# Kernel tuning notes

Measured on AMD Instinct MI355X. Metric: run time of the kernel, lower is better.

## Reference

```python
import jax, jax.numpy as jnp
import numpy as np

B, DIN, F, H, C = 8192, 2048, 2048, 2048, 345
EPS = 1e-5


def setup_inputs() -> dict:
    key = jax.random.key(0)
    ks = jax.random.split(key, 8)
    rng = np.random.default_rng(0)
    # labels and sort order (torch.sort is stable here via argsort kind='stable')
    y_np = rng.integers(0, C, size=B).astype(np.int64)
    order_np = np.argsort(y_np, kind='stable')
    ys = y_np[order_np]
    # per-class random permutations within each sorted segment (torch.randperm per interval)
    shuf1 = np.empty(B, dtype=np.int64)
    shuf2 = np.empty(B, dtype=np.int64)
    for c in np.unique(ys):
        idx = np.nonzero(ys == c)[0]
        shuf1[idx] = rng.permutation(idx)
        shuf2[idx] = rng.permutation(idx)
    s = 0.02  # weight init scale
    return {
        'x': jax.random.normal(ks[0], (B, DIN), jnp.float32),
        'lam': jnp.array([float(rng.beta(0.5, 0.5))], jnp.float32),
        'Wf': jax.random.normal(ks[1], (DIN, F), jnp.float32) * s,
        'bf': jnp.zeros((F,), jnp.float32),
        'W1': jax.random.normal(ks[2], (F, H), jnp.float32) * s,
        'b1': jnp.zeros((H,), jnp.float32),
        'g1': jnp.ones((H,), jnp.float32),
        'be1': jnp.zeros((H,), jnp.float32),
        'W2': jax.random.normal(ks[3], (H, H), jnp.float32) * s,
        'b2': jnp.zeros((H,), jnp.float32),
        'g2': jnp.ones((H,), jnp.float32),
        'be2': jnp.zeros((H,), jnp.float32),
        'W3': jax.random.normal(ks[4], (H, F), jnp.float32) * s,
        'b3': jnp.zeros((F,), jnp.float32),
        'g3': jnp.ones((F,), jnp.float32),
        'be3': jnp.zeros((F,), jnp.float32),
        'Wc': jax.random.normal(ks[5], (F, C), jnp.float32) * s,
        'bc': jnp.zeros((C,), jnp.float32),
        'y': jnp.asarray(y_np),
        'order': jnp.asarray(order_np),
        'shuf1': jnp.asarray(shuf1),
        'shuf2': jnp.asarray(shuf2),
    }


def _bn(x, g, b):
    # BatchNorm1d, training mode: biased batch stats
    m = jnp.mean(x, axis=0)
    v = jnp.var(x, axis=0)
    return (x - m) * jax.lax.rsqrt(v + EPS) * g + b


def reference(x, lam, Wf, bf, W1, b1, g1, be1, W2, b2, g2, be2, W3, b3, g3, be3, Wc, bc, y, order, shuf1, shuf2):
    lam = lam[0]
    xs = x[order]           # sorted-by-label gather (vectorized)
    ys = y[order]
    feat = jax.nn.relu(xs @ Wf + bf)                      # featurizer
    h = jax.nn.relu(_bn(feat @ W1 + b1, g1, be1))         # cdpl projector
    h = jax.nn.relu(_bn(h @ W2 + b2, g2, be2))
    proj = _bn(h @ W3 + b3, g3, be3)
    out = feat @ Wc + bc                                  # classifier logits
    out2, feat2 = out[shuf1], proj[shuf1]                 # per-class shuffles
    out3, feat3 = out[shuf2], proj[shuf2]
    out3 = lam * out2 + (1.0 - lam) * out3
    feat3 = lam * feat2 + (1.0 - lam) * feat3
    mse = lambda a, b: jnp.mean((a - b) ** 2)
    L_ind_logit = mse(out, out2)
    L_hdl_logit = mse(out, out3)
    L_ind_feat = 0.3 * mse(proj, feat2)
    L_hdl_feat = 0.3 * mse(proj, feat3)
    logp = jax.nn.log_softmax(out, axis=-1)
    cl_loss = -jnp.mean(jnp.take_along_axis(logp, ys[:, None], axis=-1))
    C_scale = jax.lax.stop_gradient(jnp.minimum(cl_loss, 1.0))  # .item() -> constant
    loss = cl_loss + C_scale * (lam * (L_ind_logit + L_ind_feat) + (1.0 - lam) * (L_hdl_logit + L_hdl_feat))
    return loss
```

## Files before the change

### kernel.cpp

```cpp
#include <hip/hip_runtime.h>

#define NB   8192
#define NF   2048
#define NC   345
#define NCP  384
#define EPSV 1e-5f

#define SX   (5.75f / 127.0f)
#define SW   (0.115f / 127.0f)
#define SF   (5.2f / 127.0f)
#define SH   (5.75f / 127.0f)
#define ST1  (3.34f / 127.0f)
#define ST2  (3.68f / 127.0f)
#define QX   (1.0f / SX)
#define QW   (1.0f / SW)
#define QF   (1.0f / SF)
#define QH   (1.0f / SH)
#define QT1  (1.0f / ST1)
#define QT2  (1.0f / ST2)

typedef __bf16 bf16x8 __attribute__((ext_vector_type(8)));
typedef float  f32x4  __attribute__((ext_vector_type(4)));
typedef int    i32x4  __attribute__((ext_vector_type(4)));

__device__ __forceinline__ float bs2f(unsigned int u) { return __uint_as_float(u << 16); }
__device__ __forceinline__ unsigned short f2bs(float f) {
    unsigned int u = __float_as_uint(f);
    u += 0x7fffu + ((u >> 16) & 1u);
    return (unsigned short)(u >> 16);
}
__device__ __forceinline__ int q8i(float v, float iq) {
    int t = __float2int_rn(v * iq);
    return t > 127 ? 127 : (t < -127 ? -127 : t);
}

#define GLD16(g, l)                                                                     \
    __builtin_amdgcn_global_load_lds((const __attribute__((address_space(1))) void*)(g),\
                                     (__attribute__((address_space(3))) void*)(l),      \
                                     16, 0, 0)

__global__ void k_gather(const float* __restrict__ x, const int* __restrict__ order,
                         char* __restrict__ xq) {
    const int row = blockIdx.x;
    const long src = order[row];
    const float4* xr = (const float4*)(x + src * 2048);
    float4 a = xr[threadIdx.x * 2 + 0];
    float4 b = xr[threadIdx.x * 2 + 1];
    unsigned int lo = (unsigned)(q8i(a.x, QX) & 255) | ((unsigned)(q8i(a.y, QX) & 255) << 8) |
                      ((unsigned)(q8i(a.z, QX) & 255) << 16) | ((unsigned)(q8i(a.w, QX) & 255) << 24);
    unsigned int hi = (unsigned)(q8i(b.x, QX) & 255) | ((unsigned)(q8i(b.y, QX) & 255) << 8) |
                      ((unsigned)(q8i(b.z, QX) & 255) << 16) | ((unsigned)(q8i(b.w, QX) & 255) << 24);
    uint2 o; o.x = lo; o.y = hi;
    ((uint2*)(xq + (long)row * 2048))[threadIdx.x] = o;
}

__global__ void k_transpose4(const float* __restrict__ W0, const float* __restrict__ W1,
                             const float* __restrict__ W2, const float* __restrict__ W3,
                             char* __restrict__ Wt) {
    __shared__ float tile[32][33];
    const float* Wz = (blockIdx.z == 0) ? W0 : (blockIdx.z == 1) ? W1
                     : (blockIdx.z == 2) ? W2 : W3;
    char* out = Wt + (size_t)blockIdx.z * 2048 * 2048;
    const int n0 = blockIdx.x * 32, k0 = blockIdx.y * 32;
    const int tx = threadIdx.x, ty = threadIdx.y;
    #pragma unroll
    for (int i = 0; i < 32; i += 8)
        tile[ty + i][tx] = Wz[(long)(k0 + ty + i) * 2048 + n0 + tx];
    __syncthreads();
    #pragma unroll
    for (int i = 0; i < 32; i += 8)
        out[(long)(n0 + ty + i) * 2048 + k0 + tx] = (char)q8i(tile[tx][ty + i], QW);
}

__global__ void k_transposeC(const float* __restrict__ W, char* __restrict__ Wt8,
                             int K, int N, int Npad) {
    __shared__ float tile[32][33];
    const int n0 = blockIdx.x * 32, k0 = blockIdx.y * 32;
    const int tx = threadIdx.x, ty = threadIdx.y;
    #pragma unroll
    for (int i = 0; i < 32; i += 8) {
        int n = n0 + tx, k = k0 + ty + i;
        tile[ty + i][tx] = (n < N) ? W[(long)k * N + n] : 0.f;
    }
    __syncthreads();
    #pragma unroll
    for (int i = 0; i < 32; i += 8) {
        int n = n0 + ty + i, k = k0 + tx;
        if (n < Npad) Wt8[(long)n * K + k] = (char)q8i(tile[tx][ty + i], QW);
    }
}

__global__ void k_padbias(const float* __restrict__ bc, float* __restrict__ bcp) {
    const int i = threadIdx.x + blockIdx.x * blockDim.x;
    if (i < NCP) bcp[i] = (i < NC) ? bc[i] : 0.f;
}

#define BARX  do { asm volatile("" ::: "memory"); __builtin_amdgcn_s_barrier(); \
                   asm volatile("" ::: "memory"); } while (0)
#define LGKM0 asm volatile("s_waitcnt lgkmcnt(0)" ::: "memory")
#define VMW4  asm volatile("s_waitcnt vmcnt(4)" ::: "memory")
#define VMW0  asm volatile("s_waitcnt vmcnt(0)" ::: "memory")

#define RDX(u, AV, BV) do {                                                            \
    const char* A_ = &L[((u) & 3) * 32768];                                            \
    const char* B_ = A_ + 16384;                                                       \
    _Pragma("unroll") for (int m_ = 0; m_ < 8; m_++)                                   \
        AV[m_] = *(const i32x4*)&A_[(wm * 128 + m_ * 16 + frow) * 64 + slt];           \
    _Pragma("unroll") for (int n_ = 0; n_ < 4; n_++)                                   \
        BV[n_] = *(const i32x4*)&B_[(wn * 64 + n_ * 16 + frow) * 64 + slt];            \
} while (0)

#define MMX(AV, BV) do {                                                               \
    __builtin_amdgcn_s_setprio(1);                                                     \
    _Pragma("unroll") for (int n_ = 0; n_ < 4; n_++)                                   \
    _Pragma("unroll") for (int m_ = 0; m_ < 8; m_++)                                   \
        acc[m_][n_] = __builtin_amdgcn_mfma_i32_16x16x64_i8(BV[n_], AV[m_],            \
                                                            acc[m_][n_], 0, 0, 0);    \
    __builtin_amdgcn_s_setprio(0);                                                     \
} while (0)

template <int RELU, int STATS>
__global__ __launch_bounds__(512, 2) void k_gemmq(
    const char* __restrict__ A,
    const char* __restrict__ Bt,
    const float* __restrict__ bias,
    char* __restrict__ C8,
    float* __restrict__ stats,
    float S, float IQ, int N, int K) {
    __shared__ char L[4 * 32768];
    const int tid  = threadIdx.x;
    const int lane = tid & 63;
    const int wv   = tid >> 6;
    const int frow = lane & 15;
    const int kg   = lane >> 4;
    const int wm   = wv >> 2;
    const int wn   = wv & 3;
    const int slt  = (kg ^ ((frow >> 1) & 3)) * 16;

    const int id  = blockIdx.x;
    const int xcd = id & 7, kid = id >> 3;
    const int brow = (xcd * 4 + (kid & 3)) * 256;
    const int bcol = (kid >> 2) * 256;

    const char* pA[2];
    const char* pB[2];
    #pragma unroll
    for (int i = 0; i < 2; i++) {
        const int q = tid + i * 512;
        const int j = q >> 2;
        const int c = (q & 3) ^ ((j >> 1) & 3);
        pA[i] = A  + (long)(brow + j) * K + c * 16;
        pB[i] = Bt + (long)(bcol + j) * K + c * 16;
    }

    i32x4 acc[8][4];
    #pragma unroll
    for (int m = 0; m < 8; m++)
        #pragma unroll
        for (int n = 0; n < 4; n++)
            #pragma unroll
            for (int r = 0; r < 4; r++) acc[m][n][r] = 0;

    auto stage = [&](int s) {
        char* Lb = &L[(s & 3) * 32768];
        const int ko = s * 64;
        GLD16(pA[0] + ko, Lb + wv * 1024);
        GLD16(pA[1] + ko, Lb + 8192 + wv * 1024);
        GLD16(pB[0] + ko, Lb + 16384 + wv * 1024);
        GLD16(pB[1] + ko, Lb + 24576 + wv * 1024);
    };

    i32x4 avA[8], bvA[4], avB[8], bvB[4];

    stage(0); stage(1); stage(2);
    VMW4; BARX;
    RDX(0, avA, bvA);

    for (int i = 0; i < 14; i++) {
        const int t = i * 2;
        RDX(t + 1, avB, bvB); stage(t + 3); MMX(avA, bvA); VMW4; BARX;
        RDX(t + 2, avA, bvA); stage(t + 4); MMX(avB, bvB); VMW4; BARX;
    }
    RDX(29, avB, bvB); stage(31); MMX(avA, bvA); VMW4; BARX;
    RDX(30, avA, bvA); MMX(avB, bvB); VMW0; BARX;
    RDX(31, avB, bvB); MMX(avA, bvA);
    MMX(avB, bvB);

    LGKM0; BARX;
    unsigned short* Ls = (unsigned short*)L;
    const int cbase = bcol + wn * 64 + kg * 4;
    #pragma unroll
    for (int n = 0; n < 4; n++) {
        const int col = cbase + n * 16;
        const float4 bb = *(const float4*)&bias[col];
        float s0_ = 0.f, s1_ = 0.f, s2_ = 0.f, s3_ = 0.f;
        float q0_ = 0.f, q1_ = 0.f, q2_ = 0.f, q3_ = 0.f;
        const int s8 = wn * 16 + n * 4 + kg;
        const int p8 = s8 ^ frow;
        #pragma unroll
        for (int m = 0; m < 8; m++) {
            const int rloc = wm * 128 + m * 16 + frow;
            float v0 = (float)acc[m][n][0] * S + bb.x;
            float v1 = (float)acc[m][n][1] * S + bb.y;
            float v2 = (float)acc[m][n][2] * S + bb.z;
            float v3 = (float)acc[m][n][3] * S + bb.w;
            if (STATS) { s0_ += v0; q0_ += v0 * v0; s1_ += v1; q1_ += v1 * v1;
                         s2_ += v2; q2_ += v2 * v2; s3_ += v3; q3_ += v3 * v3; }
            if (RELU) { v0 = fmaxf(v0, 0.f); v1 = fmaxf(v1, 0.f);
                        v2 = fmaxf(v2, 0.f); v3 = fmaxf(v3, 0.f); }
            ushort4 st; st.x = f2bs(v0); st.y = f2bs(v1); st.z = f2bs(v2); st.w = f2bs(v3);
            *(ushort4*)&Ls[rloc * 256 + p8 * 4] = st;
        }
        if (STATS) {
            #pragma unroll
            for (int off = 1; off <= 8; off <<= 1) {
                s0_ += __shfl_xor(s0_, off); s1_ += __shfl_xor(s1_, off);
                s2_ += __shfl_xor(s2_, off); s3_ += __shfl_xor(s3_, off);
                q0_ += __shfl_xor(q0_, off); q1_ += __shfl_xor(q1_, off);
                q2_ += __shfl_xor(q2_, off); q3_ += __shfl_xor(q3_, off);
            }
            if (frow == 0) {
                atomicAdd(&stats[col + 0], s0_); atomicAdd(&stats[col + 1], s1_);
                atomicAdd(&stats[col + 2], s2_); atomicAdd(&stats[col + 3], s3_);
                atomicAdd(&stats[N + col + 0], q0_); atomicAdd(&stats[N + col + 1], q1_);
                atomicAdd(&stats[N + col + 2], q2_); atomicAdd(&stats[N + col + 3], q3_);
            }
        }
    }
    LGKM0; BARX;
    #pragma unroll
    for (int it = 0; it < 16; it++) {
        const int c  = tid + it * 512;
        const int r  = c >> 5;
        const int a  = c & 31;
        const int x  = r & 15;
        const int a2 = a ^ (x >> 1);
        uint4 v = *(const uint4*)&Ls[r * 256 + a2 * 8];
        if (x & 1) { unsigned tx_ = v.x, ty_ = v.y; v.x = v.z; v.y = v.w; v.z = tx_; v.w = ty_; }
        const long grow = brow + r;
        const int  gcol = bcol + a * 8;
        unsigned int us[8] = {v.x & 0xffffu, v.x >> 16, v.y & 0xffffu, v.y >> 16,
                              v.z & 0xffffu, v.z >> 16, v.w & 0xffffu, v.w >> 16};
        unsigned int b[8];
        #pragma unroll
        for (int j = 0; j < 8; j++) b[j] = (unsigned)(q8i(bs2f(us[j]), IQ) & 255);
        uint2 o;
        o.x = b[0] | (b[1] << 8) | (b[2] << 16) | (b[3] << 24);
        o.y = b[4] | (b[5] << 8) | (b[6] << 16) | (b[7] << 24);
        *(uint2*)&C8[grow * N + gcol] = o;
    }
}

__global__ __launch_bounds__(256) void k_gemmc(const char* __restrict__ A,
                                               const char* __restrict__ Bt,
                                               const float* __restrict__ bias,
                                               float* __restrict__ Cf,
                                               float S, int K, int ldc) {
    __shared__ char As[8192];
    __shared__ char Bs[8192];
    const int tid  = threadIdx.x;
    const int lane = tid & 63;
    const int wv   = tid >> 6;
    const int brow = blockIdx.x * 128;
    const int bcol = blockIdx.y * 128;
    const int wr   = (wv >> 1) * 64;
    const int wc   = (wv & 1) * 64;
    const int frow = lane & 15;
    const int kg   = lane >> 4;
    const int slt  = (kg ^ ((frow >> 1) & 3)) * 16;

    const char* pA[2];
    const char* pB[2];
    #pragma unroll
    for (int i = 0; i < 2; i++) {
        const int q = tid + i * 256;
        const int j = q >> 2;
        const int c = (q & 3) ^ ((j >> 1) & 3);
        pA[i] = A  + (long)(brow + j) * K + c * 16;
        pB[i] = Bt + (long)(bcol + j) * K + c * 16;
    }

    i32x4 acc[4][4];
    #pragma unroll
    for (int m = 0; m < 4; m++)
        #pragma unroll
        for (int n = 0; n < 4; n++)
            #pragma unroll
            for (int r = 0; r < 4; r++) acc[m][n][r] = 0;

    for (int kt = 0; kt < K; kt += 64) {
        GLD16(pA[0] + kt, As + wv * 1024);
        GLD16(pA[1] + kt, As + 4096 + wv * 1024);
        GLD16(pB[0] + kt, Bs + wv * 1024);
        GLD16(pB[1] + kt, Bs + 4096 + wv * 1024);
        __syncthreads();
        i32x4 av[4], bv[4];
        #pragma unroll
        for (int m = 0; m < 4; m++)
            av[m] = *(const i32x4*)&As[(wr + m * 16 + frow) * 64 + slt];
        #pragma unroll
        for (int n = 0; n < 4; n++)
            bv[n] = *(const i32x4*)&Bs[(wc + n * 16 + frow) * 64 + slt];
        #pragma unroll
        for (int m = 0; m < 4; m++)
            #pragma unroll
            for (int n = 0; n < 4; n++)
                acc[m][n] = __builtin_amdgcn_mfma_i32_16x16x64_i8(bv[n], av[m],
                                                                  acc[m][n], 0, 0, 0);
        __syncthreads();
    }
    const int r0 = brow + wr + frow;
    const int c0 = bcol + wc + kg * 4;
    #pragma unroll
    for (int n = 0; n < 4; n++) {
        const int col = c0 + n * 16;
        const float4 bb = *(const float4*)&bias[col];
        #pragma unroll
        for (int m = 0; m < 4; m++) {
            const long row = r0 + m * 16;
            float4 o;
            o.x = (float)acc[m][n][0] * S + bb.x;
            o.y = (float)acc[m][n][1] * S + bb.y;
            o.z = (float)acc[m][n][2] * S + bb.z;
            o.w = (float)acc[m][n][3] * S + bb.w;
            *(float4*)&Cf[row * ldc + col] = o;
        }
    }
}

__global__ void k_bnapplyq8(const char* __restrict__ t8, const float* __restrict__ sums,
                            const float* __restrict__ g, const float* __restrict__ be,
                            char* __restrict__ o8, float St, int ncols) {
    const long i  = ((long)blockIdx.x * blockDim.x + threadIdx.x) * 8;
    const int  c0 = (int)(i & (ncols - 1));
    float sc[8], sh[8];
    #pragma unroll
    for (int j = 0; j < 8; j++) {
        const int c = c0 + j;
        const float m   = sums[c] * (1.f / NB);
        const float var = sums[ncols + c] * (1.f / NB) - m * m;
        const float s   = rsqrtf(var + EPSV) * g[c];
        sc[j] = s * St;
        sh[j] = be[c] - m * s;
    }
    uint2 v = *(const uint2*)(t8 + i);
    unsigned int b[8];
    #pragma unroll
    for (int j = 0; j < 8; j++) {
        const unsigned int w = (j < 4) ? v.x : v.y;
        const int raw = (int)(signed char)((w >> ((j & 3) * 8)) & 0xffu);
        float val = (float)raw * sc[j] + sh[j];
        val = fmaxf(val, 0.f);
        b[j] = (unsigned)(q8i(val, QH) & 255);
    }
    uint2 o;
    o.x = b[0] | (b[1] << 8) | (b[2] << 16) | (b[3] << 24);
    o.y = b[4] | (b[5] << 8) | (b[6] << 16) | (b[7] << 24);
    *(uint2*)(o8 + i) = o;
}

__global__ __launch_bounds__(256) void k_logitloss(const float* __restrict__ out,
                            const int* __restrict__ y,
                            const int* __restrict__ order, const int* __restrict__ s1,
                            const int* __restrict__ s2, const float* __restrict__ lamp,
                            float* __restrict__ acc) {
    const int lane = threadIdx.x & 63;
    const int wv   = threadIdx.x >> 6;
    const int wid  = blockIdx.x * 4 + wv;
    const int nw   = gridDim.x * 4;
    const float lam = lamp[0];
    float ce = 0.f, d1 = 0.f, d2 = 0.f;
    for (int i = wid; i < NB; i += nw) {
        const float* o  = out + (long)i * NCP;
        const float* o2 = out + (long)s1[i] * NCP;
        const float* o3 = out + (long)s2[i] * NCP;
        float v[6];
        float mx = -1e30f;
        #pragma unroll
        for (int j = 0; j < 6; j++) {
            const int c = lane + j * 64;
            if (c < NC) {
                const float a = o[c], b = o2[c], cc = o3[c];
                const float mix = lam * b + (1.f - lam) * cc;
                v[j] = a;
                d1 += (a - b) * (a - b);
                d2 += (a - mix) * (a - mix);
                mx = fmaxf(mx, a);
            } else v[j] = -1e30f;
        }
        #pragma unroll
        for (int off = 32; off; off >>= 1) mx = fmaxf(mx, __shfl_xor(mx, off));
        float se = 0.f;
        #pragma unroll
        for (int j = 0; j < 6; j++) se += expf(v[j] - mx);
        #pragma unroll
        for (int off = 32; off; off >>= 1) se += __shfl_xor(se, off);
        if (lane == 0) {
            const int yv = y[order[i]];
            ce += mx + logf(se) - o[yv];
        }
    }
    #pragma unroll
    for (int off = 32; off; off >>= 1) {
        d1 += __shfl_xor(d1, off);
        d2 += __shfl_xor(d2, off);
    }
    __shared__ float red[4][3];
    if (lane == 0) { red[wv][0] = ce; red[wv][1] = d1; red[wv][2] = d2; }
    __syncthreads();
    if (threadIdx.x == 0) {
        atomicAdd(&acc[0], red[0][0] + red[1][0] + red[2][0] + red[3][0]);
        atomicAdd(&acc[1], red[0][1] + red[1][1] + red[2][1] + red[3][1]);
        atomicAdd(&acc[2], red[0][2] + red[1][2] + red[2][2] + red[3][2]);
    }
}

__global__ __launch_bounds__(256) void k_featloss(const char* __restrict__ t3q,
                           const float* __restrict__ sums,
                           const float* __restrict__ g, const float* __restrict__ be,
                           const int* __restrict__ s1,
                           const int* __restrict__ s2, const float* __restrict__ lamp,
                           float* __restrict__ acc) {
    const int t = threadIdx.x;
    const float lam = lamp[0];
    float sc[8], sh[8];
    #pragma unroll
    for (int j = 0; j < 8; j++) {
        const int c = t * 8 + j;
        const float m   = sums[c] * (1.f / NB);
        const float var = sums[NF + c] * (1.f / NB) - m * m;
        const float s   = rsqrtf(var + EPSV) * g[c];
        sc[j] = s * ST2;
        sh[j] = be[c] - m * s;
    }
    float d1 = 0.f, d2 = 0.f;
    for (int i = blockIdx.x; i < NB; i += gridDim.x) {
        uint2 a = ((const uint2*)(t3q + (long)i * NF))[t];
        uint2 b = ((const uint2*)(t3q + (long)s1[i] * NF))[t];
        uint2 c = ((const uint2*)(t3q + (long)s2[i] * NF))[t];
        #pragma unroll
        for (int j = 0; j < 8; j++) {
            const unsigned int wa = (j < 4) ? a.x : a.y;
            const unsigned int wb = (j < 4) ? b.x : b.y;
            const unsigned int wc_ = (j < 4) ? c.x : c.y;
            const int sh8 = (j & 3) * 8;
            float pa = (float)(int)(signed char)((wa >> sh8) & 0xffu) * sc[j] + sh[j];
            float pb = (float)(int)(signed char)((wb >> sh8) & 0xffu) * sc[j] + sh[j];
            float pc = (float)(int)(signed char)((wc_ >> sh8) & 0xffu) * sc[j] + sh[j];
            float mix = lam * pb + (1.f - lam) * pc;
            d1 += (pa - pb) * (pa - pb);
            d2 += (pa - mix) * (pa - mix);
        }
    }
    #pragma unroll
    for (int off = 32; off; off >>= 1) {
        d1 += __shfl_xor(d1, off);
        d2 += __shfl_xor(d2, off);
    }
    __shared__ float r1[4], r2[4];
    if ((t & 63) == 0) { r1[t >> 6] = d1; r2[t >> 6] = d2; }
    __syncthreads();
    if (t == 0) {
        atomicAdd(&acc[3], r1[0] + r1[1] + r1[2] + r1[3]);
        atomicAdd(&acc[4], r2[0] + r2[1] + r2[2] + r2[3]);
    }
}

__global__ void k_final(const float* __restrict__ acc, const float* __restrict__ lamp,
                        float* __restrict__ outp) {
    const float lam = lamp[0];
    const float cl  = acc[0] * (1.f / NB);
    const float Lil = acc[1] * (1.f / ((float)NB * NC));
    const float Lhl = acc[2] * (1.f / ((float)NB * NC));
    const float Lif = 0.3f * acc[3] * (1.f / ((float)NB * NF));
    const float Lhf = 0.3f * acc[4] * (1.f / ((float)NB * NF));
    const float Cs  = fminf(cl, 1.f);
    outp[0] = cl + Cs * (lam * (Lil + Lif) + (1.f - lam) * (Lhl + Lhf));
}

extern "C" void kernel_launch(void* const* d_in, const int* in_sizes, int n_in,
                              void* d_out, int out_size, void* d_ws, size_t ws_size,
                              hipStream_t stream) {
    const float* x   = (const float*)d_in[0];
    const float* lam = (const float*)d_in[1];
    const float* Wf  = (const float*)d_in[2];
    const float* bf_ = (const float*)d_in[3];
    const float* W1  = (const float*)d_in[4];
    const float* b1  = (const float*)d_in[5];
    const float* g1  = (const float*)d_in[6];
    const float* be1 = (const float*)d_in[7];
    const float* W2  = (const float*)d_in[8];
    const float* b2  = (const float*)d_in[9];
    const float* g2  = (const float*)d_in[10];
    const float* be2 = (const float*)d_in[11];
    const float* W3  = (const float*)d_in[12];
    const float* b3  = (const float*)d_in[13];
    const float* g3  = (const float*)d_in[14];
    const float* be3 = (const float*)d_in[15];
    const float* Wc  = (const float*)d_in[16];
    const float* bc  = (const float*)d_in[17];
    const int* y     = (const int*)d_in[18];
    const int* order = (const int*)d_in[19];
    const int* s1    = (const int*)d_in[20];
    const int* s2    = (const int*)d_in[21];
    float* outp = (float*)d_out;

    char* ws = (char*)d_ws;
    const size_t MB = 1024 * 1024;
    char*  R0  = ws;
    char*  R2  = ws + 16 * MB;
    char*  R3  = ws + 32 * MB;
    float* outbuf = (float*)(ws + 48 * MB);
    char*  WT  = ws + 60 * MB;
    char*  WCT8 = ws + 76 * MB;
    float* stats = (float*)(ws + 77 * MB);
    float* accs  = stats + 3 * 4096;
    float* bcp   = accs + 16;

    hipMemsetAsync(stats, 0, (3 * 4096 + 8) * sizeof(float), stream);

    dim3 tb(32, 8);
    k_transpose4<<<dim3(64, 64, 4), tb, 0, stream>>>(Wf, W1, W2, W3, WT);
    k_transposeC<<<dim3(12, 64), tb, 0, stream>>>(Wc, WCT8, 2048, NC, NCP);
    k_padbias<<<2, 192, 0, stream>>>(bc, bcp);

    k_gather<<<NB, 256, 0, stream>>>(x, order, R0);

    k_gemmq<1, 0><<<256, 512, 0, stream>>>(R0, WT, bf_, R2, nullptr,
                                           SX * SW, QF, 2048, 2048);
    k_gemmc<<<dim3(64, 3), 256, 0, stream>>>(R2, WCT8, bcp, outbuf, SF * SW, 2048, NCP);
    k_gemmq<0, 1><<<256, 512, 0, stream>>>(R2, WT + 4 * MB, b1, R3, stats,
                                           SF * SW, QT1, 2048, 2048);
    k_bnapplyq8<<<8192, 256, 0, stream>>>(R3, stats, g1, be1, R0, ST1, 2048);
    k_gemmq<0, 1><<<256, 512, 0, stream>>>(R0, WT + 8 * MB, b2, R3, stats + 4096,
                                           SH * SW, QT2, 2048, 2048);
    k_bnapplyq8<<<8192, 256, 0, stream>>>(R3, stats + 4096, g2, be2, R2, ST2, 2048);
    k_gemmq<0, 1><<<256, 512, 0, stream>>>(R2, WT + 12 * MB, b3, R3, stats + 8192,
                                           SH * SW, QT2, 2048, 2048);

    k_logitloss<<<512, 256, 0, stream>>>(outbuf, y, order, s1, s2, lam, accs);
    k_featloss<<<512, 256, 0, stream>>>(R3, stats + 8192, g3, be3, s1, s2, lam, accs);
    k_final<<<1, 1, 0, stream>>>(accs, lam, outp);
}
```

Baseline: 308.4 us.

## Split-K classifier GEMM with double-buffered LDS, bf16 partials, fold bias padding

The classifier GEMM is split into two K halves over blockIdx.z, which doubles the block count from 192 to 384 to improve occupancy. Each half writes bf16 partial logits, which the logit-loss kernel sums when it reads them. The K loop now double-buffers LDS so the next tile's loads overlap the current MFMAs, and the bias-padding kernel is merged into the Wc transpose to save one launch. The cost is extra reads in the loss kernel, two partial buffers, and bf16 rounding of the logits.

```diff
diff --git a/kernel.cpp b/kernel.cpp
--- a/kernel.cpp
+++ b/kernel.cpp
@@ -73,10 +73,15 @@
 }
 
 __global__ void k_transposeC(const float* __restrict__ W, char* __restrict__ Wt8,
+                             const float* __restrict__ bc, float* __restrict__ bcp,
                              int K, int N, int Npad) {
     __shared__ float tile[32][33];
     const int n0 = blockIdx.x * 32, k0 = blockIdx.y * 32;
     const int tx = threadIdx.x, ty = threadIdx.y;
+    if (blockIdx.x == 0 && blockIdx.y == 0) {
+        const int idx = ty * 32 + tx;
+        for (int i = idx; i < Npad; i += 256) bcp[i] = (i < N) ? bc[i] : 0.f;
+    }
     #pragma unroll
     for (int i = 0; i < 32; i += 8) {
         int n = n0 + tx, k = k0 + ty + i;
@@ -88,11 +93,6 @@
         int n = n0 + ty + i, k = k0 + tx;
         if (n < Npad) Wt8[(long)n * K + k] = (char)q8i(tile[tx][ty + i], QW);
     }
-}
-
-__global__ void k_padbias(const float* __restrict__ bc, float* __restrict__ bcp) {
-    const int i = threadIdx.x + blockIdx.x * blockDim.x;
-    if (i < NCP) bcp[i] = (i < NC) ? bc[i] : 0.f;
 }
 
 #define BARX  do { asm volatile("" ::: "memory"); __builtin_amdgcn_s_barrier(); \
@@ -254,15 +254,17 @@
 __global__ __launch_bounds__(256) void k_gemmc(const char* __restrict__ A,
                                                const char* __restrict__ Bt,
                                                const float* __restrict__ bias,
-                                               float* __restrict__ Cf,
-                                               float S, int K, int ldc) {
-    __shared__ char As[8192];
-    __shared__ char Bs[8192];
+                                               unsigned short* __restrict__ outP,
+                                               float S, int K) {
+    __shared__ char As[2][8192];
+    __shared__ char Bs[2][8192];
     const int tid  = threadIdx.x;
     const int lane = tid & 63;
     const int wv   = tid >> 6;
     const int brow = blockIdx.x * 128;
     const int bcol = blockIdx.y * 128;
+    const int kz   = blockIdx.z;
+    const long k0  = (long)kz * 1024;
     const int wr   = (wv >> 1) * 64;
     const int wc   = (wv & 1) * 64;
     const int frow = lane & 15;
@@ -276,8 +278,8 @@
         const int q = tid + i * 256;
         const int j = q >> 2;
         const int c = (q & 3) ^ ((j >> 1) & 3);
-        pA[i] = A  + (long)(brow + j) * K + c * 16;
-        pB[i] = Bt + (long)(bcol + j) * K + c * 16;
+        pA[i] = A  + (long)(brow + j) * K + k0 + c * 16;
+        pB[i] = Bt + (long)(bcol + j) * K + k0 + c * 16;
     }
 
     i32x4 acc[4][4];
@@ -288,19 +290,25 @@
             #pragma unroll
             for (int r = 0; r < 4; r++) acc[m][n][r] = 0;
 
-    for (int kt = 0; kt < K; kt += 64) {
-        GLD16(pA[0] + kt, As + wv * 1024);
-        GLD16(pA[1] + kt, As + 4096 + wv * 1024);
-        GLD16(pB[0] + kt, Bs + wv * 1024);
-        GLD16(pB[1] + kt, Bs + 4096 + wv * 1024);
-        __syncthreads();
+    auto stage = [&](int t, int b) {
+        GLD16(pA[0] + t * 64, As[b] + wv * 1024);
+        GLD16(pA[1] + t * 64, As[b] + 4096 + wv * 1024);
+        GLD16(pB[0] + t * 64, Bs[b] + wv * 1024);
+        GLD16(pB[1] + t * 64, Bs[b] + 4096 + wv * 1024);
+    };
+
+    stage(0, 0);
+    __syncthreads();
+    for (int t = 0; t < 16; t++) {
+        if (t < 15) stage(t + 1, (t + 1) & 1);
+        const int b = t & 1;
         i32x4 av[4], bv[4];
         #pragma unroll
         for (int m = 0; m < 4; m++)
-            av[m] = *(const i32x4*)&As[(wr + m * 16 + frow) * 64 + slt];
+            av[m] = *(const i32x4*)&As[b][(wr + m * 16 + frow) * 64 + slt];
         #pragma unroll
         for (int n = 0; n < 4; n++)
-            bv[n] = *(const i32x4*)&Bs[(wc + n * 16 + frow) * 64 + slt];
+            bv[n] = *(const i32x4*)&Bs[b][(wc + n * 16 + frow) * 64 + slt];
         #pragma unroll
         for (int m = 0; m < 4; m++)
             #pragma unroll
@@ -311,19 +319,21 @@
     }
     const int r0 = brow + wr + frow;
     const int c0 = bcol + wc + kg * 4;
+    unsigned short* oz = outP + (long)kz * NB * NCP;
     #pragma unroll
     for (int n = 0; n < 4; n++) {
         const int col = c0 + n * 16;
-        const float4 bb = *(const float4*)&bias[col];
+        float4 bb = {0.f, 0.f, 0.f, 0.f};
+        if (kz == 0) bb = *(const float4*)&bias[col];
         #pragma unroll
         for (int m = 0; m < 4; m++) {
             const long row = r0 + m * 16;
-            float4 o;
-            o.x = (float)acc[m][n][0] * S + bb.x;
-            o.y = (float)acc[m][n][1] * S + bb.y;
-            o.z = (float)acc[m][n][2] * S + bb.z;
-            o.w = (float)acc[m][n][3] * S + bb.w;
-            *(float4*)&Cf[row * ldc + col] = o;
+            ushort4 st;
+            st.x = f2bs((float)acc[m][n][0] * S + bb.x);
+            st.y = f2bs((float)acc[m][n][1] * S + bb.y);
+            st.z = f2bs((float)acc[m][n][2] * S + bb.z);
+            st.w = f2bs((float)acc[m][n][3] * S + bb.w);
+            *(ushort4*)&oz[row * NCP + col] = st;
         }
     }
 }
@@ -359,7 +369,7 @@
     *(uint2*)(o8 + i) = o;
 }
 
-__global__ __launch_bounds__(256) void k_logitloss(const float* __restrict__ out,
+__global__ __launch_bounds__(256) void k_logitloss(const unsigned short* __restrict__ outP,
                             const int* __restrict__ y,
                             const int* __restrict__ order, const int* __restrict__ s1,
                             const int* __restrict__ s2, const float* __restrict__ lamp,
@@ -369,18 +379,21 @@
     const int wid  = blockIdx.x * 4 + wv;
     const int nw   = gridDim.x * 4;
     const float lam = lamp[0];
+    const unsigned short* P1 = outP + (long)NB * NCP;
     float ce = 0.f, d1 = 0.f, d2 = 0.f;
     for (int i = wid; i < NB; i += nw) {
-        const float* o  = out + (long)i * NCP;
-        const float* o2 = out + (long)s1[i] * NCP;
-        const float* o3 = out + (long)s2[i] * NCP;
+        const long r0 = (long)i * NCP;
+        const long r2 = (long)s1[i] * NCP;
+        const long r3 = (long)s2[i] * NCP;
         float v[6];
         float mx = -1e30f;
         #pragma unroll
         for (int j = 0; j < 6; j++) {
             const int c = lane + j * 64;
             if (c < NC) {
-                const float a = o[c], b = o2[c], cc = o3[c];
+                const float a  = bs2f(outP[r0 + c]) + bs2f(P1[r0 + c]);
+                const float b  = bs2f(outP[r2 + c]) + bs2f(P1[r2 + c]);
+                const float cc = bs2f(outP[r3 + c]) + bs2f(P1[r3 + c]);
                 const float mix = lam * b + (1.f - lam) * cc;
                 v[j] = a;
                 d1 += (a - b) * (a - b);
@@ -397,7 +410,8 @@
         for (int off = 32; off; off >>= 1) se += __shfl_xor(se, off);
         if (lane == 0) {
             const int yv = y[order[i]];
-            ce += mx + logf(se) - o[yv];
+            const float oy = bs2f(outP[r0 + yv]) + bs2f(P1[r0 + yv]);
+            ce += mx + logf(se) - oy;
         }
     }
     #pragma unroll
@@ -510,7 +524,7 @@
     char*  R0  = ws;
     char*  R2  = ws + 16 * MB;
     char*  R3  = ws + 32 * MB;
-    float* outbuf = (float*)(ws + 48 * MB);
+    unsigned short* outP = (unsigned short*)(ws + 48 * MB);
     char*  WT  = ws + 60 * MB;
     char*  WCT8 = ws + 76 * MB;
     float* stats = (float*)(ws + 77 * MB);
@@ -521,14 +535,13 @@
 
     dim3 tb(32, 8);
     k_transpose4<<<dim3(64, 64, 4), tb, 0, stream>>>(Wf, W1, W2, W3, WT);
-    k_transposeC<<<dim3(12, 64), tb, 0, stream>>>(Wc, WCT8, 2048, NC, NCP);
-    k_padbias<<<2, 192, 0, stream>>>(bc, bcp);
+    k_transposeC<<<dim3(12, 64), tb, 0, stream>>>(Wc, WCT8, bc, bcp, 2048, NC, NCP);
 
     k_gather<<<NB, 256, 0, stream>>>(x, order, R0);
 
     k_gemmq<1, 0><<<256, 512, 0, stream>>>(R0, WT, bf_, R2, nullptr,
                                            SX * SW, QF, 2048, 2048);
-    k_gemmc<<<dim3(64, 3), 256, 0, stream>>>(R2, WCT8, bcp, outbuf, SF * SW, 2048, NCP);
+    k_gemmc<<<dim3(64, 3, 2), 256, 0, stream>>>(R2, WCT8, bcp, outP, SF * SW, 2048);
     k_gemmq<0, 1><<<256, 512, 0, stream>>>(R2, WT + 4 * MB, b1, R3, stats,
                                            SF * SW, QT1, 2048, 2048);
     k_bnapplyq8<<<8192, 256, 0, stream>>>(R3, stats, g1, be1, R0, ST1, 2048);
@@ -538,7 +551,7 @@
     k_gemmq<0, 1><<<256, 512, 0, stream>>>(R2, WT + 12 * MB, b3, R3, stats + 8192,
                                            SH * SW, QT2, 2048, 2048);
 
-    k_logitloss<<<512, 256, 0, stream>>>(outbuf, y, order, s1, s2, lam, accs);
+    k_logitloss<<<512, 256, 0, stream>>>(outP, y, order, s1, s2, lam, accs);
     k_featloss<<<512, 256, 0, stream>>>(R3, stats + 8192, g3, be3, s1, s2, lam, accs);
     k_final<<<1, 1, 0, stream>>>(accs, lam, outp);
 }
```

New measurement: 301.0 us. 2.4% less time.
